# Kernel tuning notes

Hardware: AMD Instinct MI355X
Metric: run time of the kernel (lower is better)

The kernel has to match this reference:

```python
import jax, jax.numpy as jnp
import numpy as np

N_NODES = 50000
N_EDGES = 800000
H = 128
IN_DIM = 512
N_LAYERS = 3
LN_EPS = 1e-5


def setup_inputs() -> dict:
    key = jax.random.key(0)
    ks = jax.random.split(key, 12)
    s_in = 1.0 / np.sqrt(IN_DIM)
    s_h = 1.0 / np.sqrt(H)
    return {
        "peptide_feature": jax.random.normal(ks[0], (N_NODES, IN_DIM), jnp.float32),
        "proj_W": jax.random.uniform(ks[1], (IN_DIM, H), jnp.float32, -s_in, s_in),
        "proj_b": jax.random.uniform(ks[2], (H,), jnp.float32, -s_in, s_in),
        "edge_emb": jax.random.normal(ks[3], (100, H), jnp.float32),
        "conv_W1": jax.random.uniform(ks[4], (N_LAYERS, H, H), jnp.float32, -s_h, s_h),
        "conv_b1": jax.random.uniform(ks[5], (N_LAYERS, H), jnp.float32, -s_h, s_h),
        "conv_W2": jax.random.uniform(ks[6], (N_LAYERS, H, H), jnp.float32, -s_h, s_h),
        "conv_b2": jax.random.uniform(ks[7], (N_LAYERS, H), jnp.float32, -s_h, s_h),
        "ln_gamma": jnp.ones((H,), jnp.float32),
        "ln_beta": jnp.zeros((H,), jnp.float32),
        "edge_index": jax.random.randint(ks[8], (2, N_EDGES), 0, N_NODES, jnp.int64 if jax.config.jax_enable_x64 else jnp.int32),
        "edge_attr": jax.random.randint(ks[9], (N_EDGES, 1), 0, 100, jnp.int64 if jax.config.jax_enable_x64 else jnp.int32),
    }


def reference(peptide_feature, proj_W, proj_b, edge_emb, conv_W1, conv_b1,
              conv_W2, conv_b2, ln_gamma, ln_beta, edge_index, edge_attr):
    # aanet_proj: Linear(512, H)
    x = peptide_feature @ proj_W + proj_b  # [N, H]
    # edge type embedding lookup
    ea = edge_emb[edge_attr[:, 0]]  # [E, H]
    src, dst = edge_index[0], edge_index[1]
    n = x.shape[0]
    for i in range(N_LAYERS):
        # GINEConv (eps=0): aggr_i = sum_{(j->i)} relu(x_j + e_ji); out = MLP(x + aggr)
        msg = jax.nn.relu(x[src] + ea)  # [E, H] gather + add + relu
        agg = jax.ops.segment_sum(msg, dst, num_segments=n)  # scatter-add [N, H]
        h = x + agg
        h = jax.nn.relu(h @ conv_W1[i] + conv_b1[i]) @ conv_W2[i] + conv_b2[i]
        x = h + x  # residual
    # LayerNorm over last dim
    mu = jnp.mean(x, axis=-1, keepdims=True)
    var = jnp.var(x, axis=-1, keepdims=True)
    return ln_gamma * (x - mu) * jax.lax.rsqrt(var + LN_EPS) + ln_beta
```

## Files before the change

kernel.cpp:

```cpp
#include <hip/hip_runtime.h>
#include <hip/hip_bf16.h>

#define N_NODES 50000
#define N_EDGES 800000
#define H 128
#define IN_DIM 512
#define N_LAYERS 3
#define LN_EPS 1e-5f
#define SCAN_B ((N_NODES + 255) / 256)
#define BIN_CH 8192
#define BIN_BLOCKS ((N_EDGES + BIN_CH - 1) / BIN_CH)

typedef __attribute__((ext_vector_type(4))) float f32x4;
typedef __attribute__((ext_vector_type(8))) short short8;

__device__ inline ushort f2bfu(float f) {
    __hip_bfloat16 h = __float2bfloat16(f);
    return __builtin_bit_cast(ushort, h);
}
__device__ inline float bfu2f(ushort u) {
    uint v = ((uint)u) << 16;
    return __builtin_bit_cast(float, v);
}
__device__ inline float lobf(uint u) { return __builtin_bit_cast(float, u << 16); }
__device__ inline float hibf(uint u) { return __builtin_bit_cast(float, u & 0xffff0000u); }

#define SWZ(row, byte) ((byte) ^ (((row) & 7) << 4))

__device__ inline short8 cvt8(float4 a, float4 b) {
    short8 v;
    v[0] = (short)f2bfu(a.x); v[1] = (short)f2bfu(a.y);
    v[2] = (short)f2bfu(a.z); v[3] = (short)f2bfu(a.w);
    v[4] = (short)f2bfu(b.x); v[5] = (short)f2bfu(b.y);
    v[6] = (short)f2bfu(b.z); v[7] = (short)f2bfu(b.w);
    return v;
}


__global__ void hist_k(const int* __restrict__ dst, int* __restrict__ deg) {
    int e = blockIdx.x * 256 + threadIdx.x;
    if (e < N_EDGES) atomicAdd(&deg[dst[e]], 1);
}

__global__ __launch_bounds__(256) void blocksum_k(const int* __restrict__ deg,
                                                  int* __restrict__ bsum) {
    int i = blockIdx.x * 256 + threadIdx.x;
    int v = (i < N_NODES) ? deg[i] : 0;
    #pragma unroll
    for (int d = 1; d < 64; d <<= 1) v += __shfl_xor(v, d);
    __shared__ int ws[4];
    if ((threadIdx.x & 63) == 0) ws[threadIdx.x >> 6] = v;
    __syncthreads();
    if (threadIdx.x == 0) bsum[blockIdx.x] = ws[0] + ws[1] + ws[2] + ws[3];
}

__global__ __launch_bounds__(256) void scanb_k(const int* __restrict__ bsum,
                                               int* __restrict__ boff) {
    __shared__ int s[256];
    int t = threadIdx.x;
    int v = (t < SCAN_B) ? bsum[t] : 0;
    s[t] = v;
    __syncthreads();
    for (int d = 1; d < 256; d <<= 1) {
        int u = (t >= d) ? s[t - d] : 0;
        __syncthreads();
        s[t] += u;
        __syncthreads();
    }
    boff[t] = s[t] - v;
}

__global__ __launch_bounds__(256) void offs_k(const int* __restrict__ deg,
                                              const int* __restrict__ boff,
                                              int* __restrict__ offs,
                                              int* __restrict__ bbase,
                                              int* __restrict__ bcur) {
    int i = blockIdx.x * 256 + threadIdx.x;
    int lane = threadIdx.x & 63, w = threadIdx.x >> 6;
    int v = (i < N_NODES) ? deg[i] : 0;
    int inc = v;
    #pragma unroll
    for (int d = 1; d < 64; d <<= 1) {
        int u = __shfl_up(inc, d);
        if (lane >= d) inc += u;
    }
    __shared__ int wsum[4];
    if (lane == 63) wsum[w] = inc;
    __syncthreads();
    int wo = 0;
    #pragma unroll
    for (int k = 0; k < 4; k++) if (k < w) wo += wsum[k];
    int exc = boff[blockIdx.x] + wo + inc - v;
    if (i < N_NODES) offs[i] = exc;
    if ((i & 255) == 0 && i < N_NODES) { bbase[i >> 8] = exc; bcur[i >> 8] = exc; }
    if (i == N_NODES - 1) { offs[N_NODES] = exc + v; bbase[SCAN_B] = exc + v; }
}


__global__ __launch_bounds__(256) void binpass_k(const int* __restrict__ src,
                                                 const int* __restrict__ dst,
                                                 const int* __restrict__ attr,
                                                 int* __restrict__ bcur,
                                                 int* __restrict__ tmp_ep,
                                                 ushort* __restrict__ tmp_dst) {
    __shared__ int cnt[SCAN_B];
    __shared__ int lofs[SCAN_B];
    __shared__ int gbase[SCAN_B];
    __shared__ int cnt2[SCAN_B];
    __shared__ int scan_s[256];
    __shared__ int stage_ep[BIN_CH];
    __shared__ ushort stage_dst[BIN_CH];
    int tid = threadIdx.x;
    int e0 = blockIdx.x * BIN_CH;

    if (tid < SCAN_B) { cnt[tid] = 0; cnt2[tid] = 0; }
    __syncthreads();

    #pragma unroll
    for (int k = 0; k < BIN_CH / 256; k++) {
        int e = e0 + k * 256 + tid;
        if (e < N_EDGES) atomicAdd(&cnt[dst[e] >> 8], 1);
    }
    __syncthreads();

    int v = (tid < SCAN_B) ? cnt[tid] : 0;
    scan_s[tid] = v;
    __syncthreads();
    for (int d = 1; d < 256; d <<= 1) {
        int u = (tid >= d) ? scan_s[tid - d] : 0;
        __syncthreads();
        scan_s[tid] += u;
        __syncthreads();
    }
    if (tid < SCAN_B) lofs[tid] = scan_s[tid] - v;
    int total = scan_s[255];

    if (tid < SCAN_B && v > 0) gbase[tid] = atomicAdd(&bcur[tid], v);
    __syncthreads();

    #pragma unroll
    for (int k = 0; k < BIN_CH / 256; k++) {
        int e = e0 + k * 256 + tid;
        if (e < N_EDGES) {
            int d = dst[e];
            int b = d >> 8;
            int loc = lofs[b] + atomicAdd(&cnt2[b], 1);
            stage_ep[loc] = src[e] | (attr[e] << 16);
            stage_dst[loc] = (ushort)d;
        }
    }
    __syncthreads();

    for (int i = tid; i < total; i += 256) {
        ushort d = stage_dst[i];
        int b = d >> 8;
        int gp = gbase[b] + (i - lofs[b]);
        tmp_ep[gp] = stage_ep[i];
        tmp_dst[gp] = d;
    }
}


__global__ __launch_bounds__(256) void finepass_k(const int* __restrict__ tmp_ep,
                                                  const ushort* __restrict__ tmp_dst,
                                                  const int* __restrict__ offs,
                                                  const int* __restrict__ bbase,
                                                  int* __restrict__ epack) {
    __shared__ int cur[256];
    int tid = threadIdx.x;
    int node0 = blockIdx.x << 8;
    int node = node0 + tid;
    cur[tid] = (node < N_NODES) ? offs[node] : 0;
    __syncthreads();
    int lo = bbase[blockIdx.x], hi = bbase[blockIdx.x + 1];
    for (int i = lo + tid; i < hi; i += 256) {
        ushort d = tmp_dst[i];
        int ep = tmp_ep[i];
        int pos = atomicAdd(&cur[d & 255], 1);
        epack[pos] = ep;
    }
}


__global__ __launch_bounds__(256) void prep_w_k(const float* __restrict__ pW,
                                                const float* __restrict__ W1,
                                                const float* __restrict__ W2,
                                                const float* __restrict__ emb,
                                                short* __restrict__ Wt,
                                                short* __restrict__ W1t,
                                                short* __restrict__ W2t,
                                                ushort* __restrict__ embb,
                                                int* __restrict__ deg) {
    int i = blockIdx.x * 256 + threadIdx.x;
    if (i < 128 * 512) {
        int n = i >> 9, k = i & 511;
        Wt[i] = (short)f2bfu(pW[k * 128 + n]);
    }
    if (i < 3 * 128 * 128) {
        int l = i >> 14, rem = i & 16383, n = rem >> 7, k = rem & 127;
        W1t[i] = (short)f2bfu(W1[l * 16384 + k * 128 + n]);
        W2t[i] = (short)f2bfu(W2[l * 16384 + k * 128 + n]);
    }
    if (i < 100 * 128) embb[i] = f2bfu(emb[i]);
    if (i < N_NODES) deg[i] = 0;
}


__global__ __launch_bounds__(512) void proj_k(const float* __restrict__ pep,
                                              const short* __restrict__ Wt,
                                              const float* __restrict__ b,
                                              float* __restrict__ xf,
                                              ushort* __restrict__ xb) {
    __shared__ short SW[128 * 512];
    int tid = threadIdx.x, lane = tid & 63, wid = tid >> 6;

    #pragma unroll
    for (int c = 0; c < 16; c++) {
        int ch = tid + c * 512;
        int row = ch >> 6, kc = (ch & 63) * 16;
        short8 w = *(const short8*)((const char*)Wt + row * 1024 + kc);
        *(short8*)((char*)SW + SWZ(row, row * 1024 + kc)) = w;
    }
    __syncthreads();

    int m0 = blockIdx.x * 256 + wid * 32;

    const float* arow[2];
    #pragma unroll
    for (int mi = 0; mi < 2; mi++) {
        int node = m0 + mi * 16 + (lane & 15);
        if (node > N_NODES - 1) node = N_NODES - 1;
        arow[mi] = pep + (size_t)node * IN_DIM + ((lane >> 4) << 3);
    }

    f32x4 acc[2][8] = {};
    float4 A0[2][2], A1[2][2];
    #pragma unroll
    for (int mi = 0; mi < 2; mi++) {
        A0[mi][0] = *(const float4*)(arow[mi]);
        A0[mi][1] = *(const float4*)(arow[mi] + 4);
        A1[mi][0] = *(const float4*)(arow[mi] + 32);
        A1[mi][1] = *(const float4*)(arow[mi] + 36);
    }

    #pragma unroll
    for (int ks = 0; ks < 16; ks += 2) {
        {
            short8 af0 = cvt8(A0[0][0], A0[0][1]);
            short8 af1 = cvt8(A0[1][0], A0[1][1]);
            if (ks + 2 < 16) {
                #pragma unroll
                for (int mi = 0; mi < 2; mi++) {
                    A0[mi][0] = *(const float4*)(arow[mi] + (ks + 2) * 32);
                    A0[mi][1] = *(const float4*)(arow[mi] + (ks + 2) * 32 + 4);
                }
            }
            int kb2 = (ks * 32 + ((lane >> 4) << 3)) * 2;
            #pragma unroll
            for (int ni = 0; ni < 8; ni++) {
                int n = ni * 16 + (lane & 15);
                short8 bf = *(const short8*)((const char*)SW + SWZ(n, n * 1024 + kb2));
                acc[0][ni] = __builtin_amdgcn_mfma_f32_16x16x32_bf16(af0, bf, acc[0][ni], 0, 0, 0);
                acc[1][ni] = __builtin_amdgcn_mfma_f32_16x16x32_bf16(af1, bf, acc[1][ni], 0, 0, 0);
            }
        }
        {
            short8 af0 = cvt8(A1[0][0], A1[0][1]);
            short8 af1 = cvt8(A1[1][0], A1[1][1]);
            if (ks + 3 < 16) {
                #pragma unroll
                for (int mi = 0; mi < 2; mi++) {
                    A1[mi][0] = *(const float4*)(arow[mi] + (ks + 3) * 32);
                    A1[mi][1] = *(const float4*)(arow[mi] + (ks + 3) * 32 + 4);
                }
            }
            int kb2 = ((ks + 1) * 32 + ((lane >> 4) << 3)) * 2;
            #pragma unroll
            for (int ni = 0; ni < 8; ni++) {
                int n = ni * 16 + (lane & 15);
                short8 bf = *(const short8*)((const char*)SW + SWZ(n, n * 1024 + kb2));
                acc[0][ni] = __builtin_amdgcn_mfma_f32_16x16x32_bf16(af0, bf, acc[0][ni], 0, 0, 0);
                acc[1][ni] = __builtin_amdgcn_mfma_f32_16x16x32_bf16(af1, bf, acc[1][ni], 0, 0, 0);
            }
        }
    }

    #pragma unroll
    for (int ni = 0; ni < 8; ni++) {
        int col = ni * 16 + (lane & 15);
        float bb = b[col];
        #pragma unroll
        for (int mi = 0; mi < 2; mi++) {
            int rowb = m0 + mi * 16 + ((lane >> 4) << 2);
            #pragma unroll
            for (int r = 0; r < 4; r++) {
                int node = rowb + r;
                if (node < N_NODES) {
                    float v = acc[mi][ni][r] + bb;
                    xf[(size_t)node * H + col] = v;
                    xb[(size_t)node * H + col] = f2bfu(v);
                }
            }
        }
    }
}


__global__ __launch_bounds__(256) void gather_k(const ushort* __restrict__ xb,
                                                const int* __restrict__ offs,
                                                const int* __restrict__ epack,
                                                const ushort* __restrict__ embb,
                                                ushort* __restrict__ aggb) {
    int node = (blockIdx.x * 256 + threadIdx.x) >> 6;
    int lane = threadIdx.x & 63;
    if (node >= N_NODES) return;
    int beg = offs[node], end = offs[node + 1];
    float ax = 0.f, ay = 0.f;
    for (int base = beg; base < end; base += 64) {
        int myp = (base + lane < end) ? epack[base + lane] : 0;
        int cnt = min(64, end - base);
        int j = 0;
        for (; j + 4 <= cnt; j += 4) {
            int p0 = __shfl(myp, j), p1 = __shfl(myp, j + 1);
            int p2 = __shfl(myp, j + 2), p3 = __shfl(myp, j + 3);
            uint x0 = *(const uint*)(xb + (size_t)(p0 & 0xffff) * H + lane * 2);
            uint e0 = *(const uint*)(embb + (size_t)(p0 >> 16) * H + lane * 2);
            uint x1 = *(const uint*)(xb + (size_t)(p1 & 0xffff) * H + lane * 2);
            uint e1 = *(const uint*)(embb + (size_t)(p1 >> 16) * H + lane * 2);
            uint x2 = *(const uint*)(xb + (size_t)(p2 & 0xffff) * H + lane * 2);
            uint e2 = *(const uint*)(embb + (size_t)(p2 >> 16) * H + lane * 2);
            uint x3 = *(const uint*)(xb + (size_t)(p3 & 0xffff) * H + lane * 2);
            uint e3 = *(const uint*)(embb + (size_t)(p3 >> 16) * H + lane * 2);
            ax += fmaxf(lobf(x0) + lobf(e0), 0.f);
            ay += fmaxf(hibf(x0) + hibf(e0), 0.f);
            ax += fmaxf(lobf(x1) + lobf(e1), 0.f);
            ay += fmaxf(hibf(x1) + hibf(e1), 0.f);
            ax += fmaxf(lobf(x2) + lobf(e2), 0.f);
            ay += fmaxf(hibf(x2) + hibf(e2), 0.f);
            ax += fmaxf(lobf(x3) + lobf(e3), 0.f);
            ay += fmaxf(hibf(x3) + hibf(e3), 0.f);
        }
        for (; j < cnt; j++) {
            int p = __shfl(myp, j);
            uint xv = *(const uint*)(xb + (size_t)(p & 0xffff) * H + lane * 2);
            uint ev = *(const uint*)(embb + (size_t)(p >> 16) * H + lane * 2);
            ax += fmaxf(lobf(xv) + lobf(ev), 0.f);
            ay += fmaxf(hibf(xv) + hibf(ev), 0.f);
        }
    }
    uint packed = (uint)f2bfu(ax) | ((uint)f2bfu(ay) << 16);
    *(uint*)(aggb + (size_t)node * H + lane * 2) = packed;
}


#define MLP_ROWS 64
__global__ __launch_bounds__(256) void mlp_k(float* __restrict__ xf,
                                             ushort* __restrict__ xb,
                                             const ushort* __restrict__ aggb,
                                             const short* __restrict__ W1t,
                                             const float* __restrict__ b1,
                                             const short* __restrict__ W2t,
                                             const float* __restrict__ b2,
                                             const float* __restrict__ gamma,
                                             const float* __restrict__ beta,
                                             float* __restrict__ out,
                                             int write_xb, int do_ln) {
    __shared__ short S[MLP_ROWS * 128];
    __shared__ short Wb[128 * 128];
    int tid = threadIdx.x, lane = tid & 63, wid = tid >> 6;
    int wr = wid >> 1, wc = wid & 1;
    int m0 = blockIdx.x * MLP_ROWS;

    #pragma unroll
    for (int c = 0; c < 4; c++) {
        int ch = tid + c * 256;
        int row = ch >> 4, k8 = (ch & 15) * 8;
        int node = m0 + row;
        short8 hv;
        if (node < N_NODES) {
            const float* xp = xf + (size_t)node * H + k8;
            float4 x0 = *(const float4*)xp;
            float4 x1 = *(const float4*)(xp + 4);
            short8 ag = *(const short8*)(aggb + (size_t)node * H + k8);
            hv[0] = (short)f2bfu(x0.x + bfu2f((ushort)ag[0]));
            hv[1] = (short)f2bfu(x0.y + bfu2f((ushort)ag[1]));
            hv[2] = (short)f2bfu(x0.z + bfu2f((ushort)ag[2]));
            hv[3] = (short)f2bfu(x0.w + bfu2f((ushort)ag[3]));
            hv[4] = (short)f2bfu(x1.x + bfu2f((ushort)ag[4]));
            hv[5] = (short)f2bfu(x1.y + bfu2f((ushort)ag[5]));
            hv[6] = (short)f2bfu(x1.z + bfu2f((ushort)ag[6]));
            hv[7] = (short)f2bfu(x1.w + bfu2f((ushort)ag[7]));
        } else {
            hv = (short8)0;
        }
        *(short8*)((char*)S + SWZ(row, row * 256 + k8 * 2)) = hv;
    }
    #pragma unroll
    for (int c = 0; c < 8; c++) {
        int ch = tid + c * 256;
        int row = ch >> 4, k8 = (ch & 15) * 8;
        short8 w = *(const short8*)(W1t + row * H + k8);
        *(short8*)((char*)Wb + SWZ(row, row * 256 + k8 * 2)) = w;
    }
    short8 wreg2[8];
    #pragma unroll
    for (int c = 0; c < 8; c++) {
        int ch = tid + c * 256;
        int row = ch >> 4, k8 = (ch & 15) * 8;
        wreg2[c] = *(const short8*)(W2t + row * H + k8);
    }
    __syncthreads();

    f32x4 a1[2][4] = {};
    #pragma unroll
    for (int ks = 0; ks < 4; ks++) {
        int kb = ks * 32 + (lane >> 4) * 8;
        short8 af[2], bfr[4];
        #pragma unroll
        for (int mi = 0; mi < 2; mi++) {
            int r = wr * 32 + mi * 16 + (lane & 15);
            af[mi] = *(const short8*)((const char*)S + SWZ(r, r * 256 + kb * 2));
        }
        #pragma unroll
        for (int ni = 0; ni < 4; ni++) {
            int n = wc * 64 + ni * 16 + (lane & 15);
            bfr[ni] = *(const short8*)((const char*)Wb + SWZ(n, n * 256 + kb * 2));
        }
        #pragma unroll
        for (int mi = 0; mi < 2; mi++)
            #pragma unroll
            for (int ni = 0; ni < 4; ni++)
                a1[mi][ni] = __builtin_amdgcn_mfma_f32_16x16x32_bf16(
                    af[mi], bfr[ni], a1[mi][ni], 0, 0, 0);
    }
    __syncthreads();

    #pragma unroll
    for (int ni = 0; ni < 4; ni++) {
        int n = wc * 64 + ni * 16 + (lane & 15);
        float bb = b1[n];
        #pragma unroll
        for (int mi = 0; mi < 2; mi++) {
            int mrow = wr * 32 + mi * 16 + ((lane >> 4) << 2);
            #pragma unroll
            for (int r = 0; r < 4; r++) {
                int m = mrow + r;
                float tv = fmaxf(a1[mi][ni][r] + bb, 0.f);
                *(ushort*)((char*)S + SWZ(m, m * 256 + n * 2)) = f2bfu(tv);
            }
        }
    }
    #pragma unroll
    for (int c = 0; c < 8; c++) {
        int ch = tid + c * 256;
        int row = ch >> 4, k8 = (ch & 15) * 8;
        *(short8*)((char*)Wb + SWZ(row, row * 256 + k8 * 2)) = wreg2[c];
    }
    __syncthreads();

    f32x4 a2[4][2] = {};
    #pragma unroll
    for (int ks = 0; ks < 4; ks++) {
        int kb = ks * 32 + (lane >> 4) * 8;
        short8 af[4], bfr[2];
        #pragma unroll
        for (int mi = 0; mi < 4; mi++) {
            int n2 = wr * 64 + mi * 16 + (lane & 15);
            af[mi] = *(const short8*)((const char*)Wb + SWZ(n2, n2 * 256 + kb * 2));
        }
        #pragma unroll
        for (int ni = 0; ni < 2; ni++) {
            int m = wc * 32 + ni * 16 + (lane & 15);
            bfr[ni] = *(const short8*)((const char*)S + SWZ(m, m * 256 + kb * 2));
        }
        #pragma unroll
        for (int mi = 0; mi < 4; mi++)
            #pragma unroll
            for (int ni = 0; ni < 2; ni++)
                a2[mi][ni] = __builtin_amdgcn_mfma_f32_16x16x32_bf16(
                    af[mi], bfr[ni], a2[mi][ni], 0, 0, 0);
    }

    if (!do_ln) {
        #pragma unroll
        for (int ni = 0; ni < 2; ni++) {
            int node = m0 + wc * 32 + ni * 16 + (lane & 15);
            if (node >= N_NODES) continue;
            #pragma unroll
            for (int mi = 0; mi < 4; mi++) {
                int n2b = wr * 64 + mi * 16 + ((lane >> 4) << 2);
                float4 xo = *(float4*)(xf + (size_t)node * H + n2b);
                float4 bb = *(const float4*)(b2 + n2b);
                float4 o;
                o.x = a2[mi][ni][0] + bb.x + xo.x;
                o.y = a2[mi][ni][1] + bb.y + xo.y;
                o.z = a2[mi][ni][2] + bb.z + xo.z;
                o.w = a2[mi][ni][3] + bb.w + xo.w;
                *(float4*)(xf + (size_t)node * H + n2b) = o;
                if (write_xb) {
                    ushort us[4] = {f2bfu(o.x), f2bfu(o.y), f2bfu(o.z), f2bfu(o.w)};
                    *(ulong*)(xb + (size_t)node * H + n2b) = *(ulong*)us;
                }
            }
        }
    } else {
        float* F = (float*)Wb;
        __syncthreads();
        #pragma unroll
        for (int ni = 0; ni < 2; ni++) {
            int nl = wc * 32 + ni * 16 + (lane & 15);
            int node = m0 + nl;
            #pragma unroll
            for (int mi = 0; mi < 4; mi++) {
                int n2b = wr * 64 + mi * 16 + ((lane >> 4) << 2);
                float4 o = {0.f, 0.f, 0.f, 0.f};
                if (node < N_NODES) {
                    float4 xo = *(float4*)(xf + (size_t)node * H + n2b);
                    float4 bb = *(const float4*)(b2 + n2b);
                    o.x = a2[mi][ni][0] + bb.x + xo.x;
                    o.y = a2[mi][ni][1] + bb.y + xo.y;
                    o.z = a2[mi][ni][2] + bb.z + xo.z;
                    o.w = a2[mi][ni][3] + bb.w + xo.w;
                }
                *(float4*)((char*)F + SWZ(nl, nl * 512 + n2b * 4)) = o;
            }
        }
        __syncthreads();
        float2 gm = ((const float2*)gamma)[lane];
        float2 bt = ((const float2*)beta)[lane];
        for (int i = 0; i < 16; i++) {
            int row = wid * 16 + i;
            int node = m0 + row;
            if (node >= N_NODES) break;
            float2 v = *(float2*)((char*)F + SWZ(row, row * 512 + lane * 8));
            float s = v.x + v.y;
            #pragma unroll
            for (int d = 1; d < 64; d <<= 1) s += __shfl_xor(s, d);
            float mu = s * (1.f / 128.f);
            float dx = v.x - mu, dy = v.y - mu;
            float q = dx * dx + dy * dy;
            #pragma unroll
            for (int d = 1; d < 64; d <<= 1) q += __shfl_xor(q, d);
            float inv = rsqrtf(q * (1.f / 128.f) + LN_EPS);
            float2 o2;
            o2.x = gm.x * dx * inv + bt.x;
            o2.y = gm.y * dy * inv + bt.y;
            ((float2*)(out + (size_t)node * H))[lane] = o2;
        }
    }
}


extern "C" void kernel_launch(void* const* d_in, const int* in_sizes, int n_in,
                              void* d_out, int out_size, void* d_ws, size_t ws_size,
                              hipStream_t stream) {
    const float* pep    = (const float*)d_in[0];
    const float* proj_W = (const float*)d_in[1];
    const float* proj_b = (const float*)d_in[2];
    const float* emb    = (const float*)d_in[3];
    const float* cW1    = (const float*)d_in[4];
    const float* cb1    = (const float*)d_in[5];
    const float* cW2    = (const float*)d_in[6];
    const float* cb2    = (const float*)d_in[7];
    const float* gamma  = (const float*)d_in[8];
    const float* beta   = (const float*)d_in[9];
    const int*   eidx   = (const int*)d_in[10];
    const int*   attr   = (const int*)d_in[11];
    const int* src = eidx;
    const int* dst = eidx + N_EDGES;

    char* w = (char*)d_ws;
    float*  xf    = (float*)w;              w += (size_t)N_NODES * H * 4;
    ushort* xb    = (ushort*)w;             w += (size_t)N_NODES * H * 2;
    ushort* aggb  = (ushort*)w;             w += (size_t)N_NODES * H * 2;
    short*  Wt    = (short*)w;              w += 128 * 512 * 2;
    short*  W1t   = (short*)w;              w += 3 * 128 * 128 * 2;
    short*  W2t   = (short*)w;              w += 3 * 128 * 128 * 2;
    ushort* embb  = (ushort*)w;             w += 100 * 128 * 2;
    int*    offs  = (int*)w;                w += (N_NODES + 16) * 4;
    int*    deg   = (int*)w;                w += (N_NODES + 16) * 4;
    int*    bsum  = (int*)w;                w += 256 * 4;
    int*    boff  = (int*)w;                w += 256 * 4;
    int*    bbase = (int*)w;                w += 256 * 4;
    int*    bcur  = (int*)w;                w += 256 * 4;
    int*    epack = (int*)w;                w += (size_t)N_EDGES * 4;
    int*    tmp_ep = (int*)w;               w += (size_t)N_EDGES * 4;
    ushort* tmp_dst = (ushort*)w;           w += (size_t)N_EDGES * 2;

    float* out = (float*)d_out;

    prep_w_k<<<256, 256, 0, stream>>>(proj_W, cW1, cW2, emb, Wt, W1t, W2t, embb, deg);
    hist_k<<<(N_EDGES + 255) / 256, 256, 0, stream>>>(dst, deg);
    blocksum_k<<<SCAN_B, 256, 0, stream>>>(deg, bsum);
    scanb_k<<<1, 256, 0, stream>>>(bsum, boff);
    offs_k<<<SCAN_B, 256, 0, stream>>>(deg, boff, offs, bbase, bcur);
    binpass_k<<<BIN_BLOCKS, 256, 0, stream>>>(src, dst, attr, bcur, tmp_ep, tmp_dst);
    finepass_k<<<SCAN_B, 256, 0, stream>>>(tmp_ep, tmp_dst, offs, bbase, epack);

    proj_k<<<(N_NODES + 255) / 256, 512, 0, stream>>>(pep, Wt, proj_b, xf, xb);

    for (int l = 0; l < N_LAYERS; l++) {
        gather_k<<<(N_NODES * 64 + 255) / 256, 256, 0, stream>>>(
            xb, offs, epack, embb, aggb);
        mlp_k<<<(N_NODES + MLP_ROWS - 1) / MLP_ROWS, 256, 0, stream>>>(
            xf, xb, aggb,
            W1t + (size_t)l * H * H, cb1 + (size_t)l * H,
            W2t + (size_t)l * H * H, cb2 + (size_t)l * H,
            gamma, beta, out,
            (l < N_LAYERS - 1) ? 1 : 0,
            (l == N_LAYERS - 1) ? 1 : 0);
    }
}
```

Before: 305.1 us.

## Replace global per-node histogram with bucket counts and per-bucket local scan

The CSR build drops the global per-node atomic histogram and its three scan kernels. Instead, a shared-memory bucket count (256-node buckets) and a single scan produce the bucket bases, and finepass computes per-node degrees and offsets locally in shared memory. This cuts kernel launches and global atomics, at the cost of finepass reading tmp_dst twice. Separately, the projection GEMM now prefetches A tiles four k-steps ahead instead of two, which uses more registers to hide more load latency.

After: 277.4 us. -9.1%, faster.

```diff
diff --git a/kernel.cpp b/kernel.cpp
--- a/kernel.cpp
+++ b/kernel.cpp
@@ -37,28 +37,28 @@
 }
 
 
-__global__ void hist_k(const int* __restrict__ dst, int* __restrict__ deg) {
-    int e = blockIdx.x * 256 + threadIdx.x;
-    if (e < N_EDGES) atomicAdd(&deg[dst[e]], 1);
-}
-
-__global__ __launch_bounds__(256) void blocksum_k(const int* __restrict__ deg,
-                                                  int* __restrict__ bsum) {
-    int i = blockIdx.x * 256 + threadIdx.x;
-    int v = (i < N_NODES) ? deg[i] : 0;
-    #pragma unroll
-    for (int d = 1; d < 64; d <<= 1) v += __shfl_xor(v, d);
-    __shared__ int ws[4];
-    if ((threadIdx.x & 63) == 0) ws[threadIdx.x >> 6] = v;
-    __syncthreads();
-    if (threadIdx.x == 0) bsum[blockIdx.x] = ws[0] + ws[1] + ws[2] + ws[3];
-}
-
-__global__ __launch_bounds__(256) void scanb_k(const int* __restrict__ bsum,
-                                               int* __restrict__ boff) {
+__global__ __launch_bounds__(256) void bucketcnt_k(const int* __restrict__ dst,
+                                                   int* __restrict__ bcnt) {
+    __shared__ int cnt[SCAN_B];
+    int tid = threadIdx.x;
+    if (tid < SCAN_B) cnt[tid] = 0;
+    __syncthreads();
+    int e0 = blockIdx.x * BIN_CH;
+    #pragma unroll
+    for (int k = 0; k < BIN_CH / 256; k++) {
+        int e = e0 + k * 256 + tid;
+        if (e < N_EDGES) atomicAdd(&cnt[dst[e] >> 8], 1);
+    }
+    __syncthreads();
+    if (tid < SCAN_B && cnt[tid] > 0) atomicAdd(&bcnt[tid], cnt[tid]);
+}
+
+__global__ __launch_bounds__(256) void scanb_k(const int* __restrict__ bcnt,
+                                               int* __restrict__ bbase,
+                                               int* __restrict__ bcur) {
     __shared__ int s[256];
     int t = threadIdx.x;
-    int v = (t < SCAN_B) ? bsum[t] : 0;
+    int v = (t < SCAN_B) ? bcnt[t] : 0;
     s[t] = v;
     __syncthreads();
     for (int d = 1; d < 256; d <<= 1) {
@@ -67,33 +67,9 @@
         s[t] += u;
         __syncthreads();
     }
-    boff[t] = s[t] - v;
-}
-
-__global__ __launch_bounds__(256) void offs_k(const int* __restrict__ deg,
-                                              const int* __restrict__ boff,
-                                              int* __restrict__ offs,
-                                              int* __restrict__ bbase,
-                                              int* __restrict__ bcur) {
-    int i = blockIdx.x * 256 + threadIdx.x;
-    int lane = threadIdx.x & 63, w = threadIdx.x >> 6;
-    int v = (i < N_NODES) ? deg[i] : 0;
-    int inc = v;
-    #pragma unroll
-    for (int d = 1; d < 64; d <<= 1) {
-        int u = __shfl_up(inc, d);
-        if (lane >= d) inc += u;
-    }
-    __shared__ int wsum[4];
-    if (lane == 63) wsum[w] = inc;
-    __syncthreads();
-    int wo = 0;
-    #pragma unroll
-    for (int k = 0; k < 4; k++) if (k < w) wo += wsum[k];
-    int exc = boff[blockIdx.x] + wo + inc - v;
-    if (i < N_NODES) offs[i] = exc;
-    if ((i & 255) == 0 && i < N_NODES) { bbase[i >> 8] = exc; bcur[i >> 8] = exc; }
-    if (i == N_NODES - 1) { offs[N_NODES] = exc + v; bbase[SCAN_B] = exc + v; }
+    int exc = s[t] - v;
+    bbase[t] = exc;
+    if (t < SCAN_B) bcur[t] = exc;
 }
 
 
@@ -163,16 +139,38 @@
 
 __global__ __launch_bounds__(256) void finepass_k(const int* __restrict__ tmp_ep,
                                                   const ushort* __restrict__ tmp_dst,
-                                                  const int* __restrict__ offs,
                                                   const int* __restrict__ bbase,
+                                                  int* __restrict__ offs,
                                                   int* __restrict__ epack) {
+    __shared__ int deg[256];
     __shared__ int cur[256];
+    __shared__ int wsum[4];
     int tid = threadIdx.x;
-    int node0 = blockIdx.x << 8;
-    int node = node0 + tid;
-    cur[tid] = (node < N_NODES) ? offs[node] : 0;
+    deg[tid] = 0;
     __syncthreads();
     int lo = bbase[blockIdx.x], hi = bbase[blockIdx.x + 1];
+    for (int i = lo + tid; i < hi; i += 256)
+        atomicAdd(&deg[tmp_dst[i] & 255], 1);
+    __syncthreads();
+    int lane = tid & 63, w = tid >> 6;
+    int v = deg[tid];
+    int inc = v;
+    #pragma unroll
+    for (int d = 1; d < 64; d <<= 1) {
+        int u = __shfl_up(inc, d);
+        if (lane >= d) inc += u;
+    }
+    if (lane == 63) wsum[w] = inc;
+    __syncthreads();
+    int wo = 0;
+    #pragma unroll
+    for (int k = 0; k < 4; k++) if (k < w) wo += wsum[k];
+    int exc = lo + wo + inc - v;
+    int node = (blockIdx.x << 8) + tid;
+    if (node < N_NODES) offs[node] = exc;
+    if (node == N_NODES - 1) offs[N_NODES] = exc + v;
+    cur[tid] = exc;
+    __syncthreads();
     for (int i = lo + tid; i < hi; i += 256) {
         ushort d = tmp_dst[i];
         int ep = tmp_ep[i];
@@ -190,7 +188,7 @@
                                                 short* __restrict__ W1t,
                                                 short* __restrict__ W2t,
                                                 ushort* __restrict__ embb,
-                                                int* __restrict__ deg) {
+                                                int* __restrict__ bcnt) {
     int i = blockIdx.x * 256 + threadIdx.x;
     if (i < 128 * 512) {
         int n = i >> 9, k = i & 511;
@@ -202,7 +200,7 @@
         W2t[i] = (short)f2bfu(W2[l * 16384 + k * 128 + n]);
     }
     if (i < 100 * 128) embb[i] = f2bfu(emb[i]);
-    if (i < N_NODES) deg[i] = 0;
+    if (i < 256) bcnt[i] = 0;
 }
 
 
@@ -234,54 +232,34 @@
     }
 
     f32x4 acc[2][8] = {};
-    float4 A0[2][2], A1[2][2];
-    #pragma unroll
-    for (int mi = 0; mi < 2; mi++) {
-        A0[mi][0] = *(const float4*)(arow[mi]);
-        A0[mi][1] = *(const float4*)(arow[mi] + 4);
-        A1[mi][0] = *(const float4*)(arow[mi] + 32);
-        A1[mi][1] = *(const float4*)(arow[mi] + 36);
-    }
-
-    #pragma unroll
-    for (int ks = 0; ks < 16; ks += 2) {
-        {
-            short8 af0 = cvt8(A0[0][0], A0[0][1]);
-            short8 af1 = cvt8(A0[1][0], A0[1][1]);
-            if (ks + 2 < 16) {
-                #pragma unroll
-                for (int mi = 0; mi < 2; mi++) {
-                    A0[mi][0] = *(const float4*)(arow[mi] + (ks + 2) * 32);
-                    A0[mi][1] = *(const float4*)(arow[mi] + (ks + 2) * 32 + 4);
-                }
+    float4 A[4][2][2];
+    #pragma unroll
+    for (int d = 0; d < 4; d++)
+        #pragma unroll
+        for (int mi = 0; mi < 2; mi++) {
+            A[d][mi][0] = *(const float4*)(arow[mi] + d * 32);
+            A[d][mi][1] = *(const float4*)(arow[mi] + d * 32 + 4);
+        }
+
+    #pragma unroll
+    for (int ks = 0; ks < 16; ks++) {
+        int d = ks & 3;
+        short8 af0 = cvt8(A[d][0][0], A[d][0][1]);
+        short8 af1 = cvt8(A[d][1][0], A[d][1][1]);
+        if (ks + 4 < 16) {
+            #pragma unroll
+            for (int mi = 0; mi < 2; mi++) {
+                A[d][mi][0] = *(const float4*)(arow[mi] + (ks + 4) * 32);
+                A[d][mi][1] = *(const float4*)(arow[mi] + (ks + 4) * 32 + 4);
             }
-            int kb2 = (ks * 32 + ((lane >> 4) << 3)) * 2;
-            #pragma unroll
-            for (int ni = 0; ni < 8; ni++) {
-                int n = ni * 16 + (lane & 15);
-                short8 bf = *(const short8*)((const char*)SW + SWZ(n, n * 1024 + kb2));
-                acc[0][ni] = __builtin_amdgcn_mfma_f32_16x16x32_bf16(af0, bf, acc[0][ni], 0, 0, 0);
-                acc[1][ni] = __builtin_amdgcn_mfma_f32_16x16x32_bf16(af1, bf, acc[1][ni], 0, 0, 0);
-            }
-        }
-        {
-            short8 af0 = cvt8(A1[0][0], A1[0][1]);
-            short8 af1 = cvt8(A1[1][0], A1[1][1]);
-            if (ks + 3 < 16) {
-                #pragma unroll
-                for (int mi = 0; mi < 2; mi++) {
-                    A1[mi][0] = *(const float4*)(arow[mi] + (ks + 3) * 32);
-                    A1[mi][1] = *(const float4*)(arow[mi] + (ks + 3) * 32 + 4);
-                }
-            }
-            int kb2 = ((ks + 1) * 32 + ((lane >> 4) << 3)) * 2;
-            #pragma unroll
-            for (int ni = 0; ni < 8; ni++) {
-                int n = ni * 16 + (lane & 15);
-                short8 bf = *(const short8*)((const char*)SW + SWZ(n, n * 1024 + kb2));
-                acc[0][ni] = __builtin_amdgcn_mfma_f32_16x16x32_bf16(af0, bf, acc[0][ni], 0, 0, 0);
-                acc[1][ni] = __builtin_amdgcn_mfma_f32_16x16x32_bf16(af1, bf, acc[1][ni], 0, 0, 0);
-            }
+        }
+        int kb2 = (ks * 32 + ((lane >> 4) << 3)) * 2;
+        #pragma unroll
+        for (int ni = 0; ni < 8; ni++) {
+            int n = ni * 16 + (lane & 15);
+            short8 bf = *(const short8*)((const char*)SW + SWZ(n, n * 1024 + kb2));
+            acc[0][ni] = __builtin_amdgcn_mfma_f32_16x16x32_bf16(af0, bf, acc[0][ni], 0, 0, 0);
+            acc[1][ni] = __builtin_amdgcn_mfma_f32_16x16x32_bf16(af1, bf, acc[1][ni], 0, 0, 0);
         }
     }
 
@@ -578,10 +556,8 @@
     short*  W2t   = (short*)w;              w += 3 * 128 * 128 * 2;
     ushort* embb  = (ushort*)w;             w += 100 * 128 * 2;
     int*    offs  = (int*)w;                w += (N_NODES + 16) * 4;
-    int*    deg   = (int*)w;                w += (N_NODES + 16) * 4;
-    int*    bsum  = (int*)w;                w += 256 * 4;
-    int*    boff  = (int*)w;                w += 256 * 4;
-    int*    bbase = (int*)w;                w += 256 * 4;
+    int*    bcnt  = (int*)w;                w += 256 * 4;
+    int*    bbase = (int*)w;                w += 260 * 4;
     int*    bcur  = (int*)w;                w += 256 * 4;
     int*    epack = (int*)w;                w += (size_t)N_EDGES * 4;
     int*    tmp_ep = (int*)w;               w += (size_t)N_EDGES * 4;
@@ -589,13 +565,11 @@
 
     float* out = (float*)d_out;
 
-    prep_w_k<<<256, 256, 0, stream>>>(proj_W, cW1, cW2, emb, Wt, W1t, W2t, embb, deg);
-    hist_k<<<(N_EDGES + 255) / 256, 256, 0, stream>>>(dst, deg);
-    blocksum_k<<<SCAN_B, 256, 0, stream>>>(deg, bsum);
-    scanb_k<<<1, 256, 0, stream>>>(bsum, boff);
-    offs_k<<<SCAN_B, 256, 0, stream>>>(deg, boff, offs, bbase, bcur);
+    prep_w_k<<<256, 256, 0, stream>>>(proj_W, cW1, cW2, emb, Wt, W1t, W2t, embb, bcnt);
+    bucketcnt_k<<<BIN_BLOCKS, 256, 0, stream>>>(dst, bcnt);
+    scanb_k<<<1, 256, 0, stream>>>(bcnt, bbase, bcur);
     binpass_k<<<BIN_BLOCKS, 256, 0, stream>>>(src, dst, attr, bcur, tmp_ep, tmp_dst);
-    finepass_k<<<SCAN_B, 256, 0, stream>>>(tmp_ep, tmp_dst, offs, bbase, epack);
+    finepass_k<<<SCAN_B, 256, 0, stream>>>(tmp_ep, tmp_dst, bbase, offs, epack);
 
     proj_k<<<(N_NODES + 255) / 256, 512, 0, stream>>>(pep, Wt, proj_b, xf, xb);
 
```
